# Kernel tuning notes

Measured on AMD Instinct MI355X. Metric: run time of the kernel, lower is better.

## Reference

```python
import jax, jax.numpy as jnp
import numpy as np

# Model dims (mamba_ssm defaults for d_model=256)
IN_DIM = 64
D_MODEL = 256
D_INNER = 512      # expand=2
D_STATE = 16
D_CONV = 4
DT_RANK = 16       # ceil(d_model/16)
N_LAYERS = 4
BATCH = 8
SEQ = 1024


def setup_inputs() -> dict:
    key = jax.random.key(0)
    ks = jax.random.split(key, 10)
    s = lambda k, shape, sc: jax.random.normal(k, shape, jnp.float32) * sc
    return {
        "x": jax.random.normal(ks[0], (BATCH, SEQ, IN_DIM), jnp.float32),
        "Wp": s(ks[1], (D_MODEL, IN_DIM), 0.1),
        "bp": jnp.zeros((D_MODEL,), jnp.float32),
        "W_in": s(ks[2], (N_LAYERS, 2 * D_INNER, D_MODEL), 0.05),
        "conv_w": s(ks[3], (N_LAYERS, D_INNER, D_CONV), 0.2),
        "conv_b": jnp.zeros((N_LAYERS, D_INNER), jnp.float32),
        "W_x": s(ks[4], (N_LAYERS, DT_RANK + 2 * D_STATE, D_INNER), 0.05),
        "W_dt": s(ks[5], (N_LAYERS, D_INNER, DT_RANK), 0.1),
        "b_dt": jnp.full((N_LAYERS, D_INNER), -4.6, jnp.float32),  # softplus -> dt ~ 0.01
        "A_log": jnp.log(jnp.broadcast_to(
            jnp.arange(1, D_STATE + 1, dtype=jnp.float32), (N_LAYERS, D_INNER, D_STATE))),
        "Dp": jnp.ones((N_LAYERS, D_INNER), jnp.float32),
        "W_out": s(ks[6], (N_LAYERS, D_MODEL, D_INNER), 0.05),
        "ln_g": jnp.ones((N_LAYERS, D_MODEL), jnp.float32),
        "ln_b": jnp.zeros((N_LAYERS, D_MODEL), jnp.float32),
        "Wf": s(ks[7], (1, D_MODEL), 0.1),
        "bf": jnp.zeros((1,), jnp.float32),
    }


def _layernorm(x, g, b):
    m = x.mean(-1, keepdims=True)
    v = x.var(-1, keepdims=True)
    return (x - m) * jax.lax.rsqrt(v + 1e-5) * g + b


def _mamba(x, W_in, cw, cb, W_x, W_dt, b_dt, A_log, Dp, W_out):
    B, L, _ = x.shape
    xz = jnp.einsum('bld,ed->ble', x, W_in)          # (B,L,2*D_INNER)
    xh, z = jnp.split(xz, 2, axis=-1)
    # causal depthwise conv1d (kernel D_CONV) + silu
    xp = jnp.pad(xh, ((0, 0), (D_CONV - 1, 0), (0, 0)))
    xc = sum(xp[:, k:k + L, :] * cw[:, k] for k in range(D_CONV)) + cb
    xc = jax.nn.silu(xc)
    # input-dependent dt, B, C
    x_dbl = jnp.einsum('bld,ed->ble', xc, W_x)
    dtr = x_dbl[..., :DT_RANK]
    Bm = x_dbl[..., DT_RANK:DT_RANK + D_STATE]       # (B,L,N)
    Cm = x_dbl[..., -D_STATE:]                       # (B,L,N)
    dt = jax.nn.softplus(jnp.einsum('blr,dr->bld', dtr, W_dt) + b_dt)
    A = -jnp.exp(A_log)                              # (D,N)
    dA = jnp.exp(dt[..., None] * A)                  # (B,L,D,N)
    dBu = dt[..., None] * Bm[:, :, None, :] * xc[..., None]
    def step(h, inp):
        dA_t, dBu_t, C_t = inp
        h = dA_t * h + dBu_t                         # (B,D,N)
        return h, jnp.einsum('bdn,bn->bd', h, C_t)
    h0 = jnp.zeros((B, D_INNER, D_STATE), x.dtype)
    _, ys = jax.lax.scan(step, h0, (dA.transpose(1, 0, 2, 3),
                                    dBu.transpose(1, 0, 2, 3),
                                    Cm.transpose(1, 0, 2)))
    y = ys.transpose(1, 0, 2) + Dp * xc              # (B,L,D)
    y = y * jax.nn.silu(z)
    return jnp.einsum('ble,de->bld', y, W_out)


def reference(x, Wp, bp, W_in, conv_w, conv_b, W_x, W_dt, b_dt, A_log, Dp, W_out, ln_g, ln_b, Wf, bf):
    h = jnp.einsum('bli,di->bld', x, Wp) + bp
    for l in range(N_LAYERS):
        y = _mamba(h, W_in[l], conv_w[l], conv_b[l], W_x[l], W_dt[l],
                   b_dt[l], A_log[l], Dp[l], W_out[l])
        h = _layernorm(y, ln_g[l], ln_b[l])          # dropout is identity at eval
    pooled = h.mean(axis=1)                          # AdaptiveAvgPool1d(1) over L
    return pooled @ Wf.T + bf
```

## Files before the change

kernel.cpp:

```cpp
#include <hip/hip_runtime.h>
#include <hip/hip_bf16.h>
#include <math.h>

#define SEQ_LEN 1024
#define BATCH_N 8
#define DMODEL 256
#define DINNER 512
#define DSTATE 16
#define DTRANK 16
#define ROWS (BATCH_N * SEQ_LEN)
#define NCHUNK 64
#define CHUNK (SEQ_LEN / NCHUNK)
#define BD 8

typedef unsigned short u16;
typedef u16 u16x8 __attribute__((ext_vector_type(8)));
typedef short bf16x8 __attribute__((ext_vector_type(8)));
typedef float f32x4 __attribute__((ext_vector_type(4)));

__device__ __forceinline__ float siluf(float x) { return x / (1.f + expf(-x)); }
__device__ __forceinline__ float softplusf(float x) {
    return fmaxf(x, 0.f) + log1pf(expf(-fabsf(x)));
}
__device__ __forceinline__ float fexpf(float x) { return __expf(x); }
__device__ __forceinline__ float softplus_fast(float x) {
    return fmaxf(x, 0.f) + __logf(1.f + __expf(-fabsf(x)));
}
__device__ __forceinline__ float silu_fast(float x) {
    return x * __builtin_amdgcn_rcpf(1.f + __expf(-x));
}
__device__ __forceinline__ u16 bf16_rne(float x) {
    unsigned u = __builtin_bit_cast(unsigned, x);
    return (u16)((u + 0x7FFFu + ((u >> 16) & 1u)) >> 16);
}
__device__ __forceinline__ void cvt_hl(float x, u16& h, u16& l) {
    unsigned u = __builtin_bit_cast(unsigned, x);
    unsigned hb = (u + 0x7FFFu + ((u >> 16) & 1u)) >> 16;
    h = (u16)hb;
    float hf = __builtin_bit_cast(float, hb << 16);
    l = bf16_rne(x - hf);
}
__device__ __forceinline__ float pair_f(u16 h, u16 l) {
    return __builtin_bit_cast(float, (unsigned)h << 16) +
           __builtin_bit_cast(float, (unsigned)l << 16);
}
__device__ __forceinline__ size_t swa(int R, int row, int c) {
    return ((size_t)(c >> 5) * R + row) * 32 + (c & 31);
}

__global__ __launch_bounds__(256) void cvt_x_swz(
    const float* __restrict__ x, u16* __restrict__ dh, u16* __restrict__ dl)
{
    int i = blockIdx.x * 256 + threadIdx.x;
    int row = i >> 6, c = i & 63;
    u16 h, l;
    cvt_hl(x[i], h, l);
    size_t sw = swa(ROWS, row, c);
    dh[sw] = h;
    dl[sw] = l;
}

#define CWT (16384 + 4 * 262144 + 4 * 32768 + 4 * 131072)
__global__ __launch_bounds__(256) void cvt_w_swz(
    const float* __restrict__ Wp, const float* __restrict__ W_in,
    const float* __restrict__ W_x, const float* __restrict__ W_out,
    u16* __restrict__ Wpb, u16* __restrict__ Wib,
    u16* __restrict__ Wxb, u16* __restrict__ Wob)
{
    long i = (long)blockIdx.x * 256 + threadIdx.x;
    if (i >= CWT) return;
    if (i < 16384) {
        int n = (int)(i >> 6), k = (int)(i & 63);
        Wpb[((k >> 5) * 256 + n) * 32 + (k & 31)] = bf16_rne(Wp[n * 64 + k]);
        return;
    }
    i -= 16384;
    if (i < 4 * 262144) {
        int l = (int)(i >> 18), r = (int)(i & 262143);
        int n = r >> 8, k = r & 255;
        Wib[l * 262144 + ((k >> 5) * 1024 + n) * 32 + (k & 31)] =
            bf16_rne(W_in[l * 262144 + n * 256 + k]);
        return;
    }
    i -= 4 * 262144;
    if (i < 4 * 32768) {
        int l = (int)(i >> 15), r = (int)(i & 32767);
        int n = r >> 9, k = r & 511;
        float v = (n < 48) ? W_x[l * 48 * 512 + n * 512 + k] : 0.f;
        Wxb[l * 32768 + ((k >> 5) * 64 + n) * 32 + (k & 31)] = bf16_rne(v);
        return;
    }
    i -= 4 * 32768;
    {
        int l = (int)(i >> 17), r = (int)(i & 131071);
        int n = r >> 9, k = r & 511;
        Wob[l * 131072 + ((k >> 5) * 256 + n) * 32 + (k & 31)] =
            bf16_rne(W_out[l * 131072 + n * 512 + k]);
    }
}

template<int EPI>
__global__ __launch_bounds__(256) void gemm_sw(
    const u16* __restrict__ Ah, const u16* __restrict__ Al,
    const u16* __restrict__ B,
    const float* __restrict__ bias, float* __restrict__ C,
    u16* __restrict__ Ch, u16* __restrict__ Cl,
    int M, int N, int Npad, int K, int ldc)
{
    const int tid  = threadIdx.x;
    const int wave = tid >> 6, lane = tid & 63;
    const int bm   = blockIdx.y * 64, bn = blockIdx.x * 64;
    const int wm   = (wave >> 1) * 32, wn = (wave & 1) * 32;
    const int fr   = lane & 15, quad = lane >> 4;

    f32x4 acc[2][2];
#pragma unroll
    for (int i = 0; i < 2; i++)
#pragma unroll
        for (int j = 0; j < 2; j++) acc[i][j] = (f32x4){0.f, 0.f, 0.f, 0.f};

    const size_t a0 = (size_t)(bm + wm + fr) * 32 + quad * 8;
    const size_t a1 = a0 + 16 * 32;
    const size_t b0 = (size_t)(bn + wn + fr) * 32 + quad * 8;
    const size_t b1 = b0 + 16 * 32;
    const size_t astep = (size_t)M * 32;
    const size_t bstep = (size_t)Npad * 32;

    const u16* pah = Ah;
    const u16* pal = Al;
    const u16* pb  = B;
#pragma unroll 2
    for (int k0 = 0; k0 < K; k0 += 32) {
        bf16x8 ah0 = *(const bf16x8*)(pah + a0);
        bf16x8 ah1 = *(const bf16x8*)(pah + a1);
        bf16x8 al0 = *(const bf16x8*)(pal + a0);
        bf16x8 al1 = *(const bf16x8*)(pal + a1);
        bf16x8 bv0 = *(const bf16x8*)(pb + b0);
        bf16x8 bv1 = *(const bf16x8*)(pb + b1);
        acc[0][0] = __builtin_amdgcn_mfma_f32_16x16x32_bf16(ah0, bv0, acc[0][0], 0, 0, 0);
        acc[0][0] = __builtin_amdgcn_mfma_f32_16x16x32_bf16(al0, bv0, acc[0][0], 0, 0, 0);
        acc[0][1] = __builtin_amdgcn_mfma_f32_16x16x32_bf16(ah0, bv1, acc[0][1], 0, 0, 0);
        acc[0][1] = __builtin_amdgcn_mfma_f32_16x16x32_bf16(al0, bv1, acc[0][1], 0, 0, 0);
        acc[1][0] = __builtin_amdgcn_mfma_f32_16x16x32_bf16(ah1, bv0, acc[1][0], 0, 0, 0);
        acc[1][0] = __builtin_amdgcn_mfma_f32_16x16x32_bf16(al1, bv0, acc[1][0], 0, 0, 0);
        acc[1][1] = __builtin_amdgcn_mfma_f32_16x16x32_bf16(ah1, bv1, acc[1][1], 0, 0, 0);
        acc[1][1] = __builtin_amdgcn_mfma_f32_16x16x32_bf16(al1, bv1, acc[1][1], 0, 0, 0);
        pah += astep; pal += astep; pb += bstep;
    }

#pragma unroll
    for (int i = 0; i < 2; i++) {
        const int r0 = bm + wm + 16 * i + quad * 4;
#pragma unroll
        for (int reg = 0; reg < 4; reg++) {
            const int row = r0 + reg;
#pragma unroll
            for (int j = 0; j < 2; j++) {
                const int col = bn + wn + 16 * j + fr;
                if (col < N) {
                    float v = acc[i][j][reg];
                    if (bias) v += bias[col];
                    if (EPI == 0) {
                        C[(size_t)row * ldc + col] = v;
                    } else {
                        u16 h, l;
                        cvt_hl(v, h, l);
                        size_t sw = swa(M, row, col);
                        Ch[sw] = h;
                        Cl[sw] = l;
                    }
                }
            }
        }
    }
}

__global__ __launch_bounds__(256) void gemm_sw128(
    const u16* __restrict__ Ah, const u16* __restrict__ Al,
    const u16* __restrict__ B, float* __restrict__ C,
    int M, int Npad, int K, int ldc)
{
    const int tid  = threadIdx.x;
    const int wave = tid >> 6, lane = tid & 63;
    const int bm   = blockIdx.y * 64, bn = blockIdx.x * 128;
    const int wm   = (wave >> 1) * 32, wn = (wave & 1) * 64;
    const int fr   = lane & 15, quad = lane >> 4;

    f32x4 acc[2][4];
#pragma unroll
    for (int i = 0; i < 2; i++)
#pragma unroll
        for (int j = 0; j < 4; j++) acc[i][j] = (f32x4){0.f, 0.f, 0.f, 0.f};

    const size_t a0 = (size_t)(bm + wm + fr) * 32 + quad * 8;
    const size_t a1 = a0 + 16 * 32;
    size_t bofs[4];
#pragma unroll
    for (int j = 0; j < 4; j++)
        bofs[j] = (size_t)(bn + wn + 16 * j + fr) * 32 + quad * 8;
    const size_t astep = (size_t)M * 32;
    const size_t bstep = (size_t)Npad * 32;

    const u16* pah = Ah;
    const u16* pal = Al;
    const u16* pb  = B;
    for (int k0 = 0; k0 < K; k0 += 32) {
        bf16x8 ah0 = *(const bf16x8*)(pah + a0);
        bf16x8 ah1 = *(const bf16x8*)(pah + a1);
        bf16x8 al0 = *(const bf16x8*)(pal + a0);
        bf16x8 al1 = *(const bf16x8*)(pal + a1);
        bf16x8 bv[4];
#pragma unroll
        for (int j = 0; j < 4; j++) bv[j] = *(const bf16x8*)(pb + bofs[j]);
#pragma unroll
        for (int j = 0; j < 4; j++) {
            acc[0][j] = __builtin_amdgcn_mfma_f32_16x16x32_bf16(ah0, bv[j], acc[0][j], 0, 0, 0);
            acc[0][j] = __builtin_amdgcn_mfma_f32_16x16x32_bf16(al0, bv[j], acc[0][j], 0, 0, 0);
            acc[1][j] = __builtin_amdgcn_mfma_f32_16x16x32_bf16(ah1, bv[j], acc[1][j], 0, 0, 0);
            acc[1][j] = __builtin_amdgcn_mfma_f32_16x16x32_bf16(al1, bv[j], acc[1][j], 0, 0, 0);
        }
        pah += astep; pal += astep; pb += bstep;
    }

#pragma unroll
    for (int i = 0; i < 2; i++) {
        const int r0 = bm + wm + 16 * i + quad * 4;
#pragma unroll
        for (int reg = 0; reg < 4; reg++) {
            float* crow = C + (size_t)(r0 + reg) * ldc;
#pragma unroll
            for (int j = 0; j < 4; j++)
                crow[bn + wn + 16 * j + fr] = acc[i][j][reg];
        }
    }
}

__global__ __launch_bounds__(256) void gemm_xdbl(
    const u16* __restrict__ Ah, const u16* __restrict__ Al,
    const u16* __restrict__ B, float* __restrict__ C)
{
    const int tid  = threadIdx.x;
    const int wave = tid >> 6, lane = tid & 63;
    const int bm   = blockIdx.x * 32;
    const int wr   = (wave >> 1) * 16;
    const int wc   = (wave & 1) * 32;
    const int fr   = lane & 15, quad = lane >> 4;

    f32x4 acc[2];
    acc[0] = (f32x4){0.f, 0.f, 0.f, 0.f};
    acc[1] = (f32x4){0.f, 0.f, 0.f, 0.f};

    const size_t a0 = (size_t)(bm + wr + fr) * 32 + quad * 8;
    const size_t b0 = (size_t)(wc + fr) * 32 + quad * 8;
    const size_t b1 = b0 + 16 * 32;
    const size_t astep = (size_t)ROWS * 32;
    const size_t bstep = (size_t)64 * 32;

    const u16* pah = Ah;
    const u16* pal = Al;
    const u16* pb  = B;
#pragma unroll 4
    for (int k0 = 0; k0 < DINNER; k0 += 32) {
        bf16x8 ah = *(const bf16x8*)(pah + a0);
        bf16x8 al = *(const bf16x8*)(pal + a0);
        bf16x8 bv0 = *(const bf16x8*)(pb + b0);
        bf16x8 bv1 = *(const bf16x8*)(pb + b1);
        acc[0] = __builtin_amdgcn_mfma_f32_16x16x32_bf16(ah, bv0, acc[0], 0, 0, 0);
        acc[0] = __builtin_amdgcn_mfma_f32_16x16x32_bf16(al, bv0, acc[0], 0, 0, 0);
        acc[1] = __builtin_amdgcn_mfma_f32_16x16x32_bf16(ah, bv1, acc[1], 0, 0, 0);
        acc[1] = __builtin_amdgcn_mfma_f32_16x16x32_bf16(al, bv1, acc[1], 0, 0, 0);
        pah += astep; pal += astep; pb += bstep;
    }

    const int r0 = bm + wr + quad * 4;
#pragma unroll
    for (int reg = 0; reg < 4; reg++) {
        const int row = r0 + reg;
#pragma unroll
        for (int j = 0; j < 2; j++) {
            const int col = wc + 16 * j + fr;
            if (col < 48) C[(size_t)row * 48 + col] = acc[j][reg];
        }
    }
}

__global__ __launch_bounds__(256) void conv_silu_k(
    const float* __restrict__ xz, const float* __restrict__ cw,
    const float* __restrict__ cb, u16* __restrict__ xch, u16* __restrict__ xcl)
{
    int idx = blockIdx.x * 256 + threadIdx.x;
    int d  = idx & (DINNER - 1);
    int rb = idx >> 9;
    int row0 = rb * 4;
    int tb = row0 & (SEQ_LEN - 1);
    float4 w = *(const float4*)(cw + d * 4);
    const float bbv = cb[d];
    const float* p = xz + (size_t)row0 * 1024 + d;
    float xm3 = 0.f, xm2 = 0.f, xm1 = 0.f;
    if (tb >= 4) { xm3 = p[-3 * 1024]; xm2 = p[-2 * 1024]; xm1 = p[-1 * 1024]; }
    float x0 = p[0], x1 = p[1024], x2 = p[2 * 1024], x3 = p[3 * 1024];
    float o[4];
    float a;
    a = bbv; a = fmaf(xm3, w.x, a); a = fmaf(xm2, w.y, a); a = fmaf(xm1, w.z, a); a = fmaf(x0, w.w, a); o[0] = a;
    a = bbv; a = fmaf(xm2, w.x, a); a = fmaf(xm1, w.y, a); a = fmaf(x0, w.z, a);  a = fmaf(x1, w.w, a); o[1] = a;
    a = bbv; a = fmaf(xm1, w.x, a); a = fmaf(x0, w.y, a);  a = fmaf(x1, w.z, a);  a = fmaf(x2, w.w, a); o[2] = a;
    a = bbv; a = fmaf(x0, w.x, a);  a = fmaf(x1, w.y, a);  a = fmaf(x2, w.z, a);  a = fmaf(x3, w.w, a); o[3] = a;
    size_t sw = swa(ROWS, row0, d);
#pragma unroll
    for (int i = 0; i < 4; i++) {
        u16 h, l;
        cvt_hl(siluf(o[i]), h, l);
        xch[sw + i * 32] = h;
        xcl[sw + i * 32] = l;
    }
}

__global__ __launch_bounds__(512, 4) void scan_k(
    u16* __restrict__ xch,
    u16* __restrict__ xcl,
    const float* __restrict__ xdbl,
    const float* __restrict__ xz,
    const float* __restrict__ A_log,
    const float* __restrict__ Dp,
    const float* __restrict__ Wdt,
    const float* __restrict__ bdt)
{
    const int tid = threadIdx.x;
    const int dl  = tid & (BD - 1);
    const int ch  = tid >> 3;
    const int b   = blockIdx.x & 7;
    const int dg  = blockIdx.x >> 3;
    const int d   = dg * BD + dl;

    __shared__ float ldsS[NCHUNK * BD * 16];
    __shared__ float ldsD[CHUNK * 512];
    __shared__ float ldsT[NCHUNK * BD];

    float wv[16];
#pragma unroll
    for (int i = 0; i < 16; i += 4) *(float4*)&wv[i] = *(const float4*)(Wdt + d * 16 + i);
    const float bb = bdt[d];

    bool pow_ok = true;
#pragma unroll
    for (int n = 0; n < 16; n++) {
        float An = -expf(A_log[d * 16 + n]);
        pow_ok = pow_ok && (fabsf(An + (float)(n + 1)) <= 1e-3f * (float)(n + 1));
    }
    const int t0 = b * SEQ_LEN + ch * CHUNK;
    const int base = (ch * BD + dl) * 16;
    const size_t xcb = ((size_t)(d >> 5) * ROWS) * 32 + (d & 31);

    float S[16];
#pragma unroll
    for (int n = 0; n < 16; n++) S[n] = 0.f;
    float sdt = 0.f;
#pragma unroll 2
    for (int t = 0; t < CHUNK; ++t) {
        const size_t row = (size_t)(t0 + t);
        const float* xr = xdbl + row * 48;
        float qv[16], Bv[16];
#pragma unroll
        for (int i = 0; i < 16; i += 4) *(float4*)&qv[i] = *(const float4*)(xr + i);
#pragma unroll
        for (int i = 0; i < 16; i += 4) *(float4*)&Bv[i] = *(const float4*)(xr + 16 + i);
        float xcv = pair_f(xch[xcb + row * 32], xcl[xcb + row * 32]);
        float s8[8];
#pragma unroll
        for (int i = 0; i < 8; i++) s8[i] = fmaf(qv[i], wv[i], qv[i + 8] * wv[i + 8]);
        float s4_0 = s8[0] + s8[4], s4_1 = s8[1] + s8[5];
        float s4_2 = s8[2] + s8[6], s4_3 = s8[3] + s8[7];
        float dot = bb + ((s4_0 + s4_2) + (s4_1 + s4_3));
        float dtv = softplus_fast(dot);
        ldsD[t * 512 + tid] = dtv;
        sdt += dtv;
        float u = dtv * xcv;
        float p[16];
        if (pow_ok) {
            float e1 = fexpf(-dtv);
            p[0] = e1;
#pragma unroll
            for (int n = 1; n < 8; n++) p[n] = p[n - 1] * e1;
            float e8 = p[7];
#pragma unroll
            for (int n = 8; n < 16; n++) p[n] = p[n - 8] * e8;
        } else {
#pragma unroll
            for (int n = 0; n < 16; n++)
                p[n] = exp2f(dtv * (-expf(A_log[d * 16 + n])) * 1.44269504f);
        }
#pragma unroll
        for (int n = 0; n < 16; n++) S[n] = fmaf(p[n], S[n], u * Bv[n]);
    }
#pragma unroll
    for (int i = 0; i < 16; i += 4) *(float4*)&ldsS[base + i] = *(float4*)&S[i];
    ldsT[tid] = sdt;
    __syncthreads();

    if (tid < BD * 16) {
        const int dd = tid >> 4;
        const int nn = tid & 15;
        const float An = -fexpf(A_log[(dg * BD + dd) * 16 + nn]);
        float h0 = 0.f;
#pragma unroll 4
        for (int c = 0; c < NCHUNK; ++c) {
            const int idx = (c * BD + dd) * 16 + nn;
            float sdtc = ldsT[c * BD + dd];
            float Sv = ldsS[idx];
            float Pv = fexpf(sdtc * An);
            ldsS[idx] = h0;
            h0 = fmaf(Pv, h0, Sv);
        }
    }
    __syncthreads();

    float h[16];
#pragma unroll
    for (int i = 0; i < 16; i += 4) *(float4*)&h[i] = *(float4*)&ldsS[base + i];
    const float Dd = Dp[d];
#pragma unroll 2
    for (int t = 0; t < CHUNK; ++t) {
        const size_t row = (size_t)(t0 + t);
        const float* xr = xdbl + row * 48;
        float Bv[16], Cv[16];
#pragma unroll
        for (int i = 0; i < 16; i += 4) *(float4*)&Bv[i] = *(const float4*)(xr + 16 + i);
#pragma unroll
        for (int i = 0; i < 16; i += 4) *(float4*)&Cv[i] = *(const float4*)(xr + 32 + i);
        float xcv = pair_f(xch[xcb + row * 32], xcl[xcb + row * 32]);
        float zv  = xz[row * 1024 + 512 + d];
        float dtv = ldsD[t * 512 + tid];
        float u = dtv * xcv;
        float p[16];
        if (pow_ok) {
            float e1 = fexpf(-dtv);
            p[0] = e1;
#pragma unroll
            for (int n = 1; n < 8; n++) p[n] = p[n - 1] * e1;
            float e8 = p[7];
#pragma unroll
            for (int n = 8; n < 16; n++) p[n] = p[n - 8] * e8;
        } else {
#pragma unroll
            for (int n = 0; n < 16; n++)
                p[n] = exp2f(dtv * (-expf(A_log[d * 16 + n])) * 1.44269504f);
        }
        float y = 0.f;
#pragma unroll
        for (int n = 0; n < 16; n++) {
            h[n] = fmaf(p[n], h[n], u * Bv[n]);
            y = fmaf(h[n], Cv[n], y);
        }
        y = fmaf(Dd, xcv, y);
        y *= silu_fast(zv);
        u16 yh, yl;
        cvt_hl(y, yh, yl);
        xch[xcb + row * 32] = yh;
        xcl[xcb + row * 32] = yl;
    }
}

__global__ __launch_bounds__(256) void ln_k(
    const float* __restrict__ X, const float* __restrict__ g,
    const float* __restrict__ b2, u16* __restrict__ Yh, u16* __restrict__ Yl)
{
    int lane = threadIdx.x & 63;
    int row = blockIdx.x * 4 + (threadIdx.x >> 6);
    const float4 v = *(const float4*)(X + (size_t)row * 256 + lane * 4);
    float s = v.x + v.y + v.z + v.w;
    float q = v.x * v.x + v.y * v.y + v.z * v.z + v.w * v.w;
#pragma unroll
    for (int o = 1; o < 64; o <<= 1) { s += __shfl_xor(s, o, 64); q += __shfl_xor(q, o, 64); }
    float mean = s * (1.f / 256.f);
    float var = q * (1.f / 256.f) - mean * mean;
    float inv = rsqrtf(var + 1e-5f);
    float4 gg = *(const float4*)(g + lane * 4);
    float4 bb = *(const float4*)(b2 + lane * 4);
    float o0 = (v.x - mean) * inv * gg.x + bb.x;
    float o1 = (v.y - mean) * inv * gg.y + bb.y;
    float o2 = (v.z - mean) * inv * gg.z + bb.z;
    float o3 = (v.w - mean) * inv * gg.w + bb.w;
    ushort4 h4, l4;
    cvt_hl(o0, h4.x, l4.x); cvt_hl(o1, h4.y, l4.y);
    cvt_hl(o2, h4.z, l4.z); cvt_hl(o3, h4.w, l4.w);
    size_t sw = swa(ROWS, row, lane * 4);
    *(ushort4*)(Yh + sw) = h4;
    *(ushort4*)(Yl + sw) = l4;
}

__global__ __launch_bounds__(256) void final1_k(
    const u16* __restrict__ Hh, const u16* __restrict__ Hl,
    const float* __restrict__ Wf, float* __restrict__ part)
{
    const int b   = blockIdx.x >> 6;
    const int ckt = blockIdx.x & 63;
    const int c   = threadIdx.x;
    const size_t cb = ((size_t)(c >> 5) * ROWS) * 32 + (c & 31);
    const int tbase = b * SEQ_LEN + ckt * 16;
    float s = 0.f;
#pragma unroll 4
    for (int t = 0; t < 16; t++) {
        size_t sw = cb + (size_t)(tbase + t) * 32;
        s += pair_f(Hh[sw], Hl[sw]);
    }
    float v = s * Wf[c];
    int lane = c & 63;
#pragma unroll
    for (int o = 1; o < 64; o <<= 1) v += __shfl_xor(v, o, 64);
    __shared__ float red[4];
    if (lane == 0) red[c >> 6] = v;
    __syncthreads();
    if (c == 0) part[blockIdx.x] = red[0] + red[1] + red[2] + red[3];
}

__global__ __launch_bounds__(512) void final2_k(
    const float* __restrict__ part, const float* __restrict__ bf,
    float* __restrict__ out)
{
    int tid = threadIdx.x;
    int b = tid >> 6, i = tid & 63;
    float v = part[b * 64 + i];
#pragma unroll
    for (int o = 1; o < 64; o <<= 1) v += __shfl_xor(v, o, 64);
    if (i == 0) out[b] = v * (1.f / 1024.f) + bf[0];
}

extern "C" void kernel_launch(void* const* d_in, const int* in_sizes, int n_in,
                              void* d_out, int out_size, void* d_ws, size_t ws_size,
                              hipStream_t stream)
{
    const float* x      = (const float*)d_in[0];
    const float* Wp     = (const float*)d_in[1];
    const float* bp     = (const float*)d_in[2];
    const float* W_in   = (const float*)d_in[3];
    const float* conv_w = (const float*)d_in[4];
    const float* conv_b = (const float*)d_in[5];
    const float* W_x    = (const float*)d_in[6];
    const float* W_dt   = (const float*)d_in[7];
    const float* b_dt   = (const float*)d_in[8];
    const float* A_log  = (const float*)d_in[9];
    const float* Dp     = (const float*)d_in[10];
    const float* W_out  = (const float*)d_in[11];
    const float* ln_g   = (const float*)d_in[12];
    const float* ln_b   = (const float*)d_in[13];
    const float* Wf     = (const float*)d_in[14];
    const float* bf     = (const float*)d_in[15];

    char* w = (char*)d_ws;
    float* bufXZ = (float*)w;            w += (size_t)ROWS * 1024 * 4;
    float* bufXD = (float*)w;            w += (size_t)ROWS * 48 * 4;
    u16* xch  = (u16*)w;                 w += (size_t)ROWS * 512 * 2;
    u16* xcl  = (u16*)w;                 w += (size_t)ROWS * 512 * 2;
    u16* hh   = (u16*)w;                 w += (size_t)ROWS * 256 * 2;
    u16* hl   = (u16*)w;                 w += (size_t)ROWS * 256 * 2;
    u16* xih  = (u16*)w;                 w += (size_t)ROWS * 64 * 2;
    u16* xil  = (u16*)w;                 w += (size_t)ROWS * 64 * 2;
    u16* Wpb  = (u16*)w;                 w += (size_t)256 * 64 * 2;
    u16* Wib  = (u16*)w;                 w += (size_t)4 * 1024 * 256 * 2;
    u16* Wxb  = (u16*)w;                 w += (size_t)4 * 64 * 512 * 2;
    u16* Wob  = (u16*)w;                 w += (size_t)4 * 256 * 512 * 2;
    float* part = (float*)w;             w += 512 * 4;
    float* bufO = bufXZ;

    dim3 blk(256);

    cvt_x_swz<<<dim3(ROWS * 64 / 256), blk, 0, stream>>>(x, xih, xil);
    cvt_w_swz<<<dim3((CWT + 255) / 256), blk, 0, stream>>>(
        Wp, W_in, W_x, W_out, Wpb, Wib, Wxb, Wob);

    gemm_sw<1><<<dim3(4, 128), blk, 0, stream>>>(xih, xil, Wpb, bp,
                                                 nullptr, hh, hl,
                                                 ROWS, DMODEL, DMODEL, 64, 0);

    for (int l = 0; l < 4; ++l) {
        const u16* Wil = Wib + (size_t)l * 1024 * 256;
        const u16* Wxl = Wxb + (size_t)l * 64 * 512;
        const u16* Wol = Wob + (size_t)l * 256 * 512;
        const float* cw  = conv_w + (size_t)l * DINNER * 4;
        const float* cb  = conv_b + (size_t)l * DINNER;
        const float* Wdt = W_dt   + (size_t)l * DINNER * DTRANK;
        const float* bdt = b_dt   + (size_t)l * DINNER;
        const float* Al  = A_log  + (size_t)l * DINNER * DSTATE;
        const float* Dl  = Dp     + (size_t)l * DINNER;
        const float* lg  = ln_g   + (size_t)l * DMODEL;
        const float* lb  = ln_b   + (size_t)l * DMODEL;

        gemm_sw128<<<dim3(8, 128), blk, 0, stream>>>(hh, hl, Wil, bufXZ,
                                                     ROWS, 1024, DMODEL, 1024);
        conv_silu_k<<<dim3(ROWS * DINNER / 4 / 256), blk, 0, stream>>>(
            bufXZ, cw, cb, xch, xcl);
        gemm_xdbl<<<dim3(ROWS / 32), blk, 0, stream>>>(xch, xcl, Wxl, bufXD);
        scan_k<<<dim3(512), dim3(512), 0, stream>>>(xch, xcl, bufXD, bufXZ,
                                                    Al, Dl, Wdt, bdt);
        gemm_sw<0><<<dim3(4, 128), blk, 0, stream>>>(xch, xcl, Wol, nullptr,
                                                     bufO, nullptr, nullptr,
                                                     ROWS, DMODEL, DMODEL, DINNER, DMODEL);
        ln_k<<<dim3(ROWS / 4), blk, 0, stream>>>(bufO, lg, lb, hh, hl);
    }

    final1_k<<<dim3(512), blk, 0, stream>>>(hh, hl, Wf, part);
    final2_k<<<dim3(1), dim3(512), 0, stream>>>(part, bf, (float*)d_out);

    (void)in_sizes; (void)n_in; (void)out_size; (void)ws_size;
}
```

Measured before the change: 539.9 us.

## Fuse out-projection GEMM with LayerNorm into one kernel per layer

Replaces the out-projection GEMM plus the separate LayerNorm kernel with a single kernel. Each 16-row block computes all 256 output columns across four waves and reduces the row statistics through shuffles and shared memory, then applies the norm and writes the split bf16 output directly. This removes the fp32 intermediate write and reread and one launch per layer. In exchange, the new GEMM uses small 16-row tiles with direct global loads and no LDS staging, so data reuse may be worse than in the old tiled GEMM.

```diff
diff --git a/kernel.cpp b/kernel.cpp
--- a/kernel.cpp
+++ b/kernel.cpp
@@ -284,6 +284,105 @@
     }
 }
 
+__global__ __launch_bounds__(256) void gemm_out_ln(
+    const u16* __restrict__ Ah, const u16* __restrict__ Al,
+    const u16* __restrict__ B,
+    const float* __restrict__ g, const float* __restrict__ b2,
+    u16* __restrict__ Yh, u16* __restrict__ Yl)
+{
+    const int tid  = threadIdx.x;
+    const int wave = tid >> 6, lane = tid & 63;
+    const int bm   = blockIdx.x * 16;
+    const int wc   = wave * 64;
+    const int fr   = lane & 15, quad = lane >> 4;
+
+    __shared__ float gb[512];
+    __shared__ float redS[4][16];
+    __shared__ float redQ[4][16];
+    if (tid < 256) { gb[tid] = g[tid]; gb[256 + tid] = b2[tid]; }
+
+    f32x4 acc[4];
+#pragma unroll
+    for (int j = 0; j < 4; j++) acc[j] = (f32x4){0.f, 0.f, 0.f, 0.f};
+
+    const size_t a0 = (size_t)(bm + fr) * 32 + quad * 8;
+    size_t bofs[4];
+#pragma unroll
+    for (int j = 0; j < 4; j++)
+        bofs[j] = (size_t)(wc + 16 * j + fr) * 32 + quad * 8;
+    const size_t astep = (size_t)ROWS * 32;
+    const size_t bstep = (size_t)DMODEL * 32;
+
+    const u16* pah = Ah;
+    const u16* pal = Al;
+    const u16* pb  = B;
+#pragma unroll 2
+    for (int k0 = 0; k0 < DINNER; k0 += 32) {
+        bf16x8 ah = *(const bf16x8*)(pah + a0);
+        bf16x8 al = *(const bf16x8*)(pal + a0);
+        bf16x8 bv[4];
+#pragma unroll
+        for (int j = 0; j < 4; j++) bv[j] = *(const bf16x8*)(pb + bofs[j]);
+#pragma unroll
+        for (int j = 0; j < 4; j++) {
+            acc[j] = __builtin_amdgcn_mfma_f32_16x16x32_bf16(ah, bv[j], acc[j], 0, 0, 0);
+            acc[j] = __builtin_amdgcn_mfma_f32_16x16x32_bf16(al, bv[j], acc[j], 0, 0, 0);
+        }
+        pah += astep; pal += astep; pb += bstep;
+    }
+
+    float s[4], q[4];
+#pragma unroll
+    for (int reg = 0; reg < 4; reg++) {
+        float ss = 0.f, qq = 0.f;
+#pragma unroll
+        for (int j = 0; j < 4; j++) {
+            float v = acc[j][reg];
+            ss += v;
+            qq = fmaf(v, v, qq);
+        }
+        s[reg] = ss; q[reg] = qq;
+    }
+#pragma unroll
+    for (int o = 1; o < 16; o <<= 1) {
+#pragma unroll
+        for (int reg = 0; reg < 4; reg++) {
+            s[reg] += __shfl_xor(s[reg], o, 64);
+            q[reg] += __shfl_xor(q[reg], o, 64);
+        }
+    }
+    __syncthreads();
+    if (fr == 0) {
+#pragma unroll
+        for (int reg = 0; reg < 4; reg++) {
+            redS[wave][quad * 4 + reg] = s[reg];
+            redQ[wave][quad * 4 + reg] = q[reg];
+        }
+    }
+    __syncthreads();
+
+#pragma unroll
+    for (int reg = 0; reg < 4; reg++) {
+        const int rl = quad * 4 + reg;
+        const int row = bm + rl;
+        float S = (redS[0][rl] + redS[1][rl]) + (redS[2][rl] + redS[3][rl]);
+        float Q = (redQ[0][rl] + redQ[1][rl]) + (redQ[2][rl] + redQ[3][rl]);
+        float mean = S * (1.f / 256.f);
+        float var  = Q * (1.f / 256.f) - mean * mean;
+        float inv  = rsqrtf(var + 1e-5f);
+#pragma unroll
+        for (int j = 0; j < 4; j++) {
+            const int col = wc + 16 * j + fr;
+            float o = (acc[j][reg] - mean) * inv * gb[col] + gb[256 + col];
+            u16 h, l;
+            cvt_hl(o, h, l);
+            size_t sw = swa(ROWS, row, col);
+            Yh[sw] = h;
+            Yl[sw] = l;
+        }
+    }
+}
+
 __global__ __launch_bounds__(256) void conv_silu_k(
     const float* __restrict__ xz, const float* __restrict__ cw,
     const float* __restrict__ cb, u16* __restrict__ xch, u16* __restrict__ xcl)
@@ -460,34 +559,6 @@
     }
 }
 
-__global__ __launch_bounds__(256) void ln_k(
-    const float* __restrict__ X, const float* __restrict__ g,
-    const float* __restrict__ b2, u16* __restrict__ Yh, u16* __restrict__ Yl)
-{
-    int lane = threadIdx.x & 63;
-    int row = blockIdx.x * 4 + (threadIdx.x >> 6);
-    const float4 v = *(const float4*)(X + (size_t)row * 256 + lane * 4);
-    float s = v.x + v.y + v.z + v.w;
-    float q = v.x * v.x + v.y * v.y + v.z * v.z + v.w * v.w;
-#pragma unroll
-    for (int o = 1; o < 64; o <<= 1) { s += __shfl_xor(s, o, 64); q += __shfl_xor(q, o, 64); }
-    float mean = s * (1.f / 256.f);
-    float var = q * (1.f / 256.f) - mean * mean;
-    float inv = rsqrtf(var + 1e-5f);
-    float4 gg = *(const float4*)(g + lane * 4);
-    float4 bb = *(const float4*)(b2 + lane * 4);
-    float o0 = (v.x - mean) * inv * gg.x + bb.x;
-    float o1 = (v.y - mean) * inv * gg.y + bb.y;
-    float o2 = (v.z - mean) * inv * gg.z + bb.z;
-    float o3 = (v.w - mean) * inv * gg.w + bb.w;
-    ushort4 h4, l4;
-    cvt_hl(o0, h4.x, l4.x); cvt_hl(o1, h4.y, l4.y);
-    cvt_hl(o2, h4.z, l4.z); cvt_hl(o3, h4.w, l4.w);
-    size_t sw = swa(ROWS, row, lane * 4);
-    *(ushort4*)(Yh + sw) = h4;
-    *(ushort4*)(Yl + sw) = l4;
-}
-
 __global__ __launch_bounds__(256) void final1_k(
     const u16* __restrict__ Hh, const u16* __restrict__ Hl,
     const float* __restrict__ Wf, float* __restrict__ part)
@@ -560,7 +631,6 @@
     u16* Wxb  = (u16*)w;                 w += (size_t)4 * 64 * 512 * 2;
     u16* Wob  = (u16*)w;                 w += (size_t)4 * 256 * 512 * 2;
     float* part = (float*)w;             w += 512 * 4;
-    float* bufO = bufXZ;
 
     dim3 blk(256);
 
@@ -592,10 +662,8 @@
         gemm_xdbl<<<dim3(ROWS / 32), blk, 0, stream>>>(xch, xcl, Wxl, bufXD);
         scan_k<<<dim3(512), dim3(512), 0, stream>>>(xch, xcl, bufXD, bufXZ,
                                                     Al, Dl, Wdt, bdt);
-        gemm_sw<0><<<dim3(4, 128), blk, 0, stream>>>(xch, xcl, Wol, nullptr,
-                                                     bufO, nullptr, nullptr,
-                                                     ROWS, DMODEL, DMODEL, DINNER, DMODEL);
-        ln_k<<<dim3(ROWS / 4), blk, 0, stream>>>(bufO, lg, lb, hh, hl);
+        gemm_out_ln<<<dim3(ROWS / 16), blk, 0, stream>>>(xch, xcl, Wol,
+                                                         lg, lb, hh, hl);
     }
 
     final1_k<<<dim3(512), blk, 0, stream>>>(hh, hl, Wf, part);
```

Result: no change. 530.3 us (-1.8%).
